# Kernel optimization log

Measured on AMD Instinct MI355X. Metric: run time of the kernel, lower is better.

## Reference

```python
import jax, jax.numpy as jnp
import numpy as np

E = 131072   # total messages
N = 8192     # dim_size (num nodes)
D = 256      # input_dim == hidden_dim (forced by h + m add)


def setup_inputs() -> dict:
    key = jax.random.key(0)
    k1, k2, k3, k4, k5 = jax.random.split(key, 5)
    msg = jax.random.normal(k1, (E, D), dtype=jnp.float32)
    index = jax.random.randint(k2, (E,), 0, N)
    t = jax.random.uniform(k3, (E,), dtype=jnp.float32)
    # torch.nn.Linear(D, D) params (kaiming-uniform-ish scale)
    W = jax.random.normal(k4, (D, D), dtype=jnp.float32) / np.sqrt(D)
    b = (jax.random.normal(k5, (D,), dtype=jnp.float32) * 0.01)
    return {"msg": msg, "index": index, "t": t, "dim_size": N, "W": W, "b": b}


def reference(msg, index, t, dim_size, W, b):
    # Original: for each node, sort its messages by t, then run the linear
    # recurrence h <- W @ (m + h) + b starting from h = 0; nodes with no
    # messages keep h = 0. Vectorized: one global stable sort by (index, t),
    # then a single segmented lax.scan with reset at segment boundaries.
    num_msgs, d = msg.shape
    order = jnp.lexsort((t, index))          # primary key: index, secondary: t
    m_sorted = msg[order]                     # [E, d]
    seg = index[order]                        # [E]

    def step(carry, inp):
        h, prev = carry
        m, s = inp
        h_in = jnp.where(s == prev, h, jnp.zeros_like(h))  # reset at new segment
        h_new = (m + h_in) @ W.T + b
        return (h_new, s), h_new

    init = (jnp.zeros((d,), msg.dtype), jnp.asarray(-1, seg.dtype))
    _, ys = jax.lax.scan(step, init, (m_sorted, seg))      # ys: [E, d]

    # final hidden per node = h at the last message of its segment
    pos = jnp.arange(num_msgs)
    last = jax.ops.segment_max(pos, seg, num_segments=dim_size)
    counts = jax.ops.segment_sum(jnp.ones((num_msgs,), jnp.int32), seg,
                                 num_segments=dim_size)
    gathered = ys[jnp.clip(last, 0, num_msgs - 1)]          # [N, d]
    hidden = jnp.where((counts > 0)[:, None], gathered, jnp.zeros_like(gathered))
    return hidden
```

## Files before the change

### kernel.cpp

```cpp
#include <hip/hip_runtime.h>
#include <hip/hip_bf16.h>

#define E_MSGS 131072
#define N_NODES 8192
#define D_DIM 256
#define XA_STRIDE 264

typedef __bf16 bf16x8 __attribute__((ext_vector_type(8)));
typedef float f32x4 __attribute__((ext_vector_type(4)));

#define BAR() asm volatile("s_waitcnt lgkmcnt(0)\n\ts_barrier" ::: "memory")


__global__ void k_scatter(const int* __restrict__ index, int* __restrict__ cursors,
                          int* __restrict__ pad) {
    int e = blockIdx.x * blockDim.x + threadIdx.x;
    int n = index[e];
    int p = atomicAdd(&cursors[n], 1);
    if (p < 64) pad[(n << 6) + p] = e;
}

__global__ void k_perm(const int* __restrict__ counts, int* __restrict__ perm) {
    __shared__ int hist[65];
    __shared__ int hcur[65];
    int tid = threadIdx.x;
    if (tid < 65) hist[tid] = 0;
    __syncthreads();
    int myc[32];
#pragma unroll
    for (int i = 0; i < 32; i++) {
        int c = min(counts[tid * 32 + i], 64);
        myc[i] = c;
        atomicAdd(&hist[c], 1);
    }
    __syncthreads();
    if (tid == 0) {
        int run = 0;
        for (int c = 64; c >= 0; c--) { hcur[c] = run; run += hist[c]; }
    }
    __syncthreads();
#pragma unroll
    for (int i = 0; i < 32; i++) {
        int pos = atomicAdd(&hcur[myc[i]], 1);
        perm[pos] = tid * 32 + i;
    }
}

__global__ void k_sortseg(const float* __restrict__ t, const int* __restrict__ counts,
                          int* __restrict__ pad) {
    int wid = (blockIdx.x * 256 + threadIdx.x) >> 6;
    int ln = threadIdx.x & 63;
    int cnt = min(counts[wid], 64);
    int base = wid << 6;
    int e = 0; float tv = 0.f;
    if (ln < cnt) { e = pad[base + ln]; tv = t[e]; }
    int rank = 0;
    for (int j = 0; j < cnt; j++) {
        float tj = __shfl(tv, j);
        int ej = __shfl(e, j);
        rank += (tj < tv) || (tj == tv && ej < e);
    }
    if (ln < cnt) pad[base + rank] = e;
}


__launch_bounds__(512, 4)
__global__ void k_gru(const float* __restrict__ msg, const float* __restrict__ W,
                      const float* __restrict__ b, const int* __restrict__ counts,
                      const int* __restrict__ spad, const int* __restrict__ perm,
                      float* __restrict__ out) {
    __shared__ __bf16 xA[2][16 * XA_STRIDE];

    int tid  = threadIdx.x;
    int wave = tid >> 6;
    int lane = tid & 63;
    int q    = lane >> 4;
    int l    = lane & 15;
    int node0 = blockIdx.x * 16;

    bf16x8 wf[8][2];
#pragma unroll
    for (int t4 = 0; t4 < 2; t4++) {
        const float* wr = W + (32 * wave + 16 * t4 + l) * D_DIM;
#pragma unroll
        for (int c = 0; c < 8; c++) {
            int k0 = 32 * c + 8 * q;
            float4 w0 = *(const float4*)(wr + k0);
            float4 w1 = *(const float4*)(wr + k0 + 4);
            bf16x8 f;
            f[0] = (__bf16)w0.x; f[1] = (__bf16)w0.y; f[2] = (__bf16)w0.z; f[3] = (__bf16)w0.w;
            f[4] = (__bf16)w1.x; f[5] = (__bf16)w1.y; f[6] = (__bf16)w1.z; f[7] = (__bf16)w1.w;
            wf[c][t4] = f;
        }
    }
    float bias[2];
#pragma unroll
    for (int t4 = 0; t4 < 2; t4++) bias[t4] = b[32 * wave + 16 * t4 + l];

    int base4[4], cnt4[4];
#pragma unroll
    for (int r = 0; r < 4; r++) {
        int n = perm[node0 + 4 * q + r];
        base4[r] = n << 6;
        cnt4[r] = min(counts[n], 64);
    }
    int S = min(counts[perm[node0]], 64);

    float h[2][4];
#pragma unroll
    for (int t4 = 0; t4 < 2; t4++)
#pragma unroll
        for (int r = 0; r < 4; r++) h[t4][r] = 0.f;

    float mvA[4][2], mvB[4][2];
    int sidp[4];
#pragma unroll
    for (int r = 0; r < 4; r++) {
        int s0 = spad[base4[r]];
        int s1 = spad[base4[r] + 1];
        const float* m0 = msg + (long)s0 * D_DIM;
        const float* m1 = msg + (long)s1 * D_DIM;
#pragma unroll
        for (int t4 = 0; t4 < 2; t4++) {
            int col = 32 * wave + 16 * t4 + l;
            xA[0][(4 * q + r) * XA_STRIDE + col] = (__bf16)m0[col];
            mvA[r][t4] = m1[col];
        }
        sidp[r] = spad[base4[r] + 2];
    }
    BAR();

    auto step = [&](int s, float (&cur)[4][2], float (&nxt)[4][2]) {
#pragma unroll
        for (int r = 0; r < 4; r++) {
            const float* mrow = msg + (long)sidp[r] * D_DIM;
#pragma unroll
            for (int t4 = 0; t4 < 2; t4++) nxt[r][t4] = mrow[32 * wave + 16 * t4 + l];
        }
#pragma unroll
        for (int r = 0; r < 4; r++)
            sidp[r] = spad[base4[r] + min(s + 3, 63)];

        const __bf16* buf = xA[s & 1];
        f32x4 acc[2];
#pragma unroll
        for (int t4 = 0; t4 < 2; t4++) acc[t4] = (f32x4){0.f, 0.f, 0.f, 0.f};
#pragma unroll
        for (int c = 0; c < 8; c++) {
            bf16x8 a = *(const bf16x8*)(buf + l * XA_STRIDE + 32 * c + 8 * q);
#pragma unroll
            for (int t4 = 0; t4 < 2; t4++)
                acc[t4] = __builtin_amdgcn_mfma_f32_16x16x32_bf16(a, wf[c][t4], acc[t4], 0, 0, 0);
        }

        __bf16* nbuf = xA[(s + 1) & 1];
#pragma unroll
        for (int t4 = 0; t4 < 2; t4++) {
#pragma unroll
            for (int r = 0; r < 4; r++) {
                float hn = acc[t4][r] + bias[t4];
                bool valid = s < cnt4[r];
                h[t4][r] = valid ? hn : h[t4][r];
                nbuf[(4 * q + r) * XA_STRIDE + 32 * wave + 16 * t4 + l] =
                    (__bf16)(h[t4][r] + cur[r][t4]);
            }
        }
        BAR();
    };

    int s = 0;
    while (s < S) {
        step(s, mvA, mvB);
        s++;
        if (s >= S) break;
        step(s, mvB, mvA);
        s++;
    }

#pragma unroll
    for (int r = 0; r < 4; r++) {
        int n = perm[node0 + 4 * q + r];
#pragma unroll
        for (int t4 = 0; t4 < 2; t4++)
            out[(long)n * D_DIM + 32 * wave + 16 * t4 + l] = h[t4][r];
    }
}


extern "C" void kernel_launch(void* const* d_in, const int* in_sizes, int n_in,
                              void* d_out, int out_size, void* d_ws, size_t ws_size,
                              hipStream_t stream) {
    const float* msg   = (const float*)d_in[0];
    const int*   index = (const int*)d_in[1];
    const float* t     = (const float*)d_in[2];
    const float* W     = (const float*)d_in[4];
    const float* b     = (const float*)d_in[5];
    float* out = (float*)d_out;

    int* ws = (int*)d_ws;
    int* cursors = ws;
    int* pad     = ws + 8192;
    int* perm    = ws + 8192 + 8192 * 64;

    hipMemsetAsync(cursors, 0, (8192 + 8192 * 64) * sizeof(int), stream);

    k_scatter<<<E_MSGS / 256, 256, 0, stream>>>(index, cursors, pad);
    k_perm<<<1, 256, 0, stream>>>(cursors, perm);
    k_sortseg<<<N_NODES * 64 / 256, 256, 0, stream>>>(t, cursors, pad);
    k_gru<<<N_NODES / 16, 512, 0, stream>>>(msg, W, b, cursors, pad, perm, out);
}
```

Measured before the change: 250.4 us.

## Unroll recurrence two steps at a time using precomputed W squared

Precomputes V = W·W and c2 = W·b + b in a prep kernel that is merged with the permutation kernel. The GRU kernel then advances two messages per step as h'' = V(h+m1) + W m2 + c2, with a prologue step for odd-length segments. This halves the number of serial barrier-separated steps along the dependency chain, in exchange for twice the MFMA work per step, double the weight registers (launch bounds lowered to 2 blocks) and extra bf16 rounding from the squared matrix.

```diff
diff --git a/kernel.cpp b/kernel.cpp
--- a/kernel.cpp
+++ b/kernel.cpp
@@ -20,29 +20,52 @@
     if (p < 64) pad[(n << 6) + p] = e;
 }
 
-__global__ void k_perm(const int* __restrict__ counts, int* __restrict__ perm) {
-    __shared__ int hist[65];
-    __shared__ int hcur[65];
+__global__ void k_prep2(const float* __restrict__ W, const float* __restrict__ b,
+                        const int* __restrict__ counts, float* __restrict__ V,
+                        float* __restrict__ c2, int* __restrict__ perm) {
     int tid = threadIdx.x;
-    if (tid < 65) hist[tid] = 0;
-    __syncthreads();
-    int myc[32];
-#pragma unroll
-    for (int i = 0; i < 32; i++) {
-        int c = min(counts[tid * 32 + i], 64);
-        myc[i] = c;
-        atomicAdd(&hist[c], 1);
-    }
-    __syncthreads();
-    if (tid == 0) {
-        int run = 0;
-        for (int c = 64; c >= 0; c--) { hcur[c] = run; run += hist[c]; }
-    }
-    __syncthreads();
-#pragma unroll
-    for (int i = 0; i < 32; i++) {
-        int pos = atomicAdd(&hcur[myc[i]], 1);
-        perm[pos] = tid * 32 + i;
+    if (blockIdx.x < 256) {
+        int i = blockIdx.x, j = tid;
+        __shared__ float red[256];
+        red[j] = W[i * 256 + j] * b[j];
+        __syncthreads();
+        for (int s = 128; s > 0; s >>= 1) {
+            if (j < s) red[j] += red[j + s];
+            __syncthreads();
+        }
+        if (j == 0) c2[i] = red[0] + b[i];
+        float acc = 0.f;
+        for (int k = 0; k < 256; k += 4) {
+            float4 wi = *(const float4*)(W + i * 256 + k);
+            acc += wi.x * W[(k + 0) * 256 + j];
+            acc += wi.y * W[(k + 1) * 256 + j];
+            acc += wi.z * W[(k + 2) * 256 + j];
+            acc += wi.w * W[(k + 3) * 256 + j];
+        }
+        V[i * 256 + j] = acc;
+    } else {
+        __shared__ int hist[65];
+        __shared__ int hcur[65];
+        if (tid < 65) hist[tid] = 0;
+        __syncthreads();
+        int myc[32];
+#pragma unroll
+        for (int i = 0; i < 32; i++) {
+            int c = min(counts[tid * 32 + i], 64);
+            myc[i] = c;
+            atomicAdd(&hist[c], 1);
+        }
+        __syncthreads();
+        if (tid == 0) {
+            int run = 0;
+            for (int c = 64; c >= 0; c--) { hcur[c] = run; run += hist[c]; }
+        }
+        __syncthreads();
+#pragma unroll
+        for (int i = 0; i < 32; i++) {
+            int pos = atomicAdd(&hcur[myc[i]], 1);
+            perm[pos] = tid * 32 + i;
+        }
     }
 }
 
@@ -64,24 +87,25 @@
 }
 
 
-__launch_bounds__(512, 4)
-__global__ void k_gru(const float* __restrict__ msg, const float* __restrict__ W,
-                      const float* __restrict__ b, const int* __restrict__ counts,
-                      const int* __restrict__ spad, const int* __restrict__ perm,
-                      float* __restrict__ out) {
-    __shared__ __bf16 xA[2][16 * XA_STRIDE];
+__launch_bounds__(512, 2)
+__global__ void k_gru2(const float* __restrict__ msg, const float* __restrict__ W,
+                       const float* __restrict__ V, const float* __restrict__ b,
+                       const float* __restrict__ c2, const int* __restrict__ counts,
+                       const int* __restrict__ spad, const int* __restrict__ perm,
+                       float* __restrict__ out) {
+    __shared__ __bf16 xB[2][16 * XA_STRIDE];
+    __shared__ __bf16 yB[2][16 * XA_STRIDE];
 
     int tid  = threadIdx.x;
-    int wave = tid >> 6;
-    int lane = tid & 63;
-    int q    = lane >> 4;
-    int l    = lane & 15;
+    int wave = tid >> 6, lane = tid & 63, q = lane >> 4, l = lane & 15;
     int node0 = blockIdx.x * 16;
-
-    bf16x8 wf[8][2];
-#pragma unroll
-    for (int t4 = 0; t4 < 2; t4++) {
-        const float* wr = W + (32 * wave + 16 * t4 + l) * D_DIM;
+    int col[2] = {32 * wave + l, 32 * wave + 16 + l};
+
+    bf16x8 wfW[8][2], wfV[8][2];
+#pragma unroll
+    for (int t = 0; t < 2; t++) {
+        const float* wr = W + (long)col[t] * D_DIM;
+        const float* vr = V + (long)col[t] * D_DIM;
 #pragma unroll
         for (int c = 0; c < 8; c++) {
             int k0 = 32 * c + 8 * q;
@@ -90,99 +114,154 @@
             bf16x8 f;
             f[0] = (__bf16)w0.x; f[1] = (__bf16)w0.y; f[2] = (__bf16)w0.z; f[3] = (__bf16)w0.w;
             f[4] = (__bf16)w1.x; f[5] = (__bf16)w1.y; f[6] = (__bf16)w1.z; f[7] = (__bf16)w1.w;
-            wf[c][t4] = f;
-        }
-    }
-    float bias[2];
-#pragma unroll
-    for (int t4 = 0; t4 < 2; t4++) bias[t4] = b[32 * wave + 16 * t4 + l];
-
-    int base4[4], cnt4[4];
+            wfW[c][t] = f;
+            float4 v0 = *(const float4*)(vr + k0);
+            float4 v1 = *(const float4*)(vr + k0 + 4);
+            bf16x8 g;
+            g[0] = (__bf16)v0.x; g[1] = (__bf16)v0.y; g[2] = (__bf16)v0.z; g[3] = (__bf16)v0.w;
+            g[4] = (__bf16)v1.x; g[5] = (__bf16)v1.y; g[6] = (__bf16)v1.z; g[7] = (__bf16)v1.w;
+            wfV[c][t] = g;
+        }
+    }
+    float bias[2]  = {b[col[0]], b[col[1]]};
+    float bias2[2] = {c2[col[0]], c2[col[1]]};
+
+    int base4[4], o4[4], dlim[4];
 #pragma unroll
     for (int r = 0; r < 4; r++) {
         int n = perm[node0 + 4 * q + r];
         base4[r] = n << 6;
-        cnt4[r] = min(counts[n], 64);
-    }
-    int S = min(counts[perm[node0]], 64);
-
+        int c = min(counts[n], 64);
+        o4[r] = c & 1;
+        dlim[r] = (c - o4[r]) >> 1;
+    }
+    int D = min(counts[perm[node0]], 64) >> 1;
+
+    float m_pro[4][2], mx0[4][2], my0[4][2], mA[4][2], mA2[4][2];
+    __bf16 mB[4][2], mB2[4][2];
+    int sidN[4][2];
+#pragma unroll
+    for (int r = 0; r < 4; r++) {
+        int o = o4[r];
+        int s_pro = spad[base4[r]];
+        int sx = spad[base4[r] + o];
+        int sy = spad[base4[r] + o + 1];
+        int sA = spad[base4[r] + o + 2];
+        int sB = spad[base4[r] + o + 3];
+        const float* mp = msg + (long)s_pro * D_DIM;
+        const float* mx = msg + (long)sx * D_DIM;
+        const float* my = msg + (long)sy * D_DIM;
+        const float* ma = msg + (long)sA * D_DIM;
+        const float* mb = msg + (long)sB * D_DIM;
+#pragma unroll
+        for (int t = 0; t < 2; t++) {
+            m_pro[r][t] = mp[col[t]];
+            mx0[r][t]   = mx[col[t]];
+            my0[r][t]   = my[col[t]];
+            mA[r][t]    = ma[col[t]];
+            mB[r][t]    = (__bf16)mb[col[t]];
+        }
+        sidN[r][0] = spad[base4[r] + min(o + 4, 63)];
+        sidN[r][1] = spad[base4[r] + min(o + 5, 63)];
+    }
+#pragma unroll
+    for (int t = 0; t < 2; t++)
+#pragma unroll
+        for (int r = 0; r < 4; r++)
+            xB[0][(4 * q + r) * XA_STRIDE + col[t]] = (__bf16)m_pro[r][t];
+    BAR();
+    f32x4 accP[2];
+#pragma unroll
+    for (int t = 0; t < 2; t++) accP[t] = (f32x4){0.f, 0.f, 0.f, 0.f};
+#pragma unroll
+    for (int c = 0; c < 8; c++) {
+        bf16x8 a = *(const bf16x8*)(&xB[0][0] + l * XA_STRIDE + 32 * c + 8 * q);
+#pragma unroll
+        for (int t = 0; t < 2; t++)
+            accP[t] = __builtin_amdgcn_mfma_f32_16x16x32_bf16(a, wfW[c][t], accP[t], 0, 0, 0);
+    }
     float h[2][4];
 #pragma unroll
-    for (int t4 = 0; t4 < 2; t4++)
-#pragma unroll
-        for (int r = 0; r < 4; r++) h[t4][r] = 0.f;
-
-    float mvA[4][2], mvB[4][2];
-    int sidp[4];
-#pragma unroll
-    for (int r = 0; r < 4; r++) {
-        int s0 = spad[base4[r]];
-        int s1 = spad[base4[r] + 1];
-        const float* m0 = msg + (long)s0 * D_DIM;
-        const float* m1 = msg + (long)s1 * D_DIM;
-#pragma unroll
-        for (int t4 = 0; t4 < 2; t4++) {
-            int col = 32 * wave + 16 * t4 + l;
-            xA[0][(4 * q + r) * XA_STRIDE + col] = (__bf16)m0[col];
-            mvA[r][t4] = m1[col];
-        }
-        sidp[r] = spad[base4[r] + 2];
-    }
+    for (int t = 0; t < 2; t++)
+#pragma unroll
+        for (int r = 0; r < 4; r++)
+            h[t][r] = o4[r] ? (accP[t][r] + bias[t]) : 0.f;
+#pragma unroll
+    for (int t = 0; t < 2; t++)
+#pragma unroll
+        for (int r = 0; r < 4; r++) {
+            xB[1][(4 * q + r) * XA_STRIDE + col[t]] = (__bf16)(h[t][r] + mx0[r][t]);
+            yB[1][(4 * q + r) * XA_STRIDE + col[t]] = (__bf16)my0[r][t];
+        }
     BAR();
 
-    auto step = [&](int s, float (&cur)[4][2], float (&nxt)[4][2]) {
+    auto dstep = [&](int d, float (&cA)[4][2], __bf16 (&cB)[4][2],
+                     float (&nA)[4][2], __bf16 (&nB)[4][2]) {
 #pragma unroll
         for (int r = 0; r < 4; r++) {
-            const float* mrow = msg + (long)sidp[r] * D_DIM;
-#pragma unroll
-            for (int t4 = 0; t4 < 2; t4++) nxt[r][t4] = mrow[32 * wave + 16 * t4 + l];
-        }
-#pragma unroll
-        for (int r = 0; r < 4; r++)
-            sidp[r] = spad[base4[r] + min(s + 3, 63)];
-
-        const __bf16* buf = xA[s & 1];
-        f32x4 acc[2];
-#pragma unroll
-        for (int t4 = 0; t4 < 2; t4++) acc[t4] = (f32x4){0.f, 0.f, 0.f, 0.f};
+            const float* ma = msg + (long)sidN[r][0] * D_DIM;
+            const float* mb = msg + (long)sidN[r][1] * D_DIM;
+#pragma unroll
+            for (int t = 0; t < 2; t++) {
+                nA[r][t] = ma[col[t]];
+                nB[r][t] = (__bf16)mb[col[t]];
+            }
+        }
+#pragma unroll
+        for (int r = 0; r < 4; r++) {
+            sidN[r][0] = spad[base4[r] + min(o4[r] + 2 * d + 6, 63)];
+            sidN[r][1] = spad[base4[r] + min(o4[r] + 2 * d + 7, 63)];
+        }
+        int rb = (d + 1) & 1, wb = d & 1;
+        f32x4 accX[2], accY[2];
+#pragma unroll
+        for (int t = 0; t < 2; t++) {
+            accX[t] = (f32x4){0.f, 0.f, 0.f, 0.f};
+            accY[t] = (f32x4){0.f, 0.f, 0.f, 0.f};
+        }
 #pragma unroll
         for (int c = 0; c < 8; c++) {
-            bf16x8 a = *(const bf16x8*)(buf + l * XA_STRIDE + 32 * c + 8 * q);
-#pragma unroll
-            for (int t4 = 0; t4 < 2; t4++)
-                acc[t4] = __builtin_amdgcn_mfma_f32_16x16x32_bf16(a, wf[c][t4], acc[t4], 0, 0, 0);
-        }
-
-        __bf16* nbuf = xA[(s + 1) & 1];
-#pragma unroll
-        for (int t4 = 0; t4 < 2; t4++) {
+            bf16x8 ax = *(const bf16x8*)(&xB[rb][0] + l * XA_STRIDE + 32 * c + 8 * q);
+#pragma unroll
+            for (int t = 0; t < 2; t++)
+                accX[t] = __builtin_amdgcn_mfma_f32_16x16x32_bf16(ax, wfV[c][t], accX[t], 0, 0, 0);
+        }
+#pragma unroll
+        for (int c = 0; c < 8; c++) {
+            bf16x8 ay = *(const bf16x8*)(&yB[rb][0] + l * XA_STRIDE + 32 * c + 8 * q);
+#pragma unroll
+            for (int t = 0; t < 2; t++)
+                accY[t] = __builtin_amdgcn_mfma_f32_16x16x32_bf16(ay, wfW[c][t], accY[t], 0, 0, 0);
+        }
+#pragma unroll
+        for (int t = 0; t < 2; t++) {
 #pragma unroll
             for (int r = 0; r < 4; r++) {
-                float hn = acc[t4][r] + bias[t4];
-                bool valid = s < cnt4[r];
-                h[t4][r] = valid ? hn : h[t4][r];
-                nbuf[(4 * q + r) * XA_STRIDE + 32 * wave + 16 * t4 + l] =
-                    (__bf16)(h[t4][r] + cur[r][t4]);
+                float hn = accX[t][r] + accY[t][r] + bias2[t];
+                bool valid = d < dlim[r];
+                h[t][r] = valid ? hn : h[t][r];
+                xB[wb][(4 * q + r) * XA_STRIDE + col[t]] = (__bf16)(h[t][r] + cA[r][t]);
+                yB[wb][(4 * q + r) * XA_STRIDE + col[t]] = cB[r][t];
             }
         }
         BAR();
     };
 
-    int s = 0;
-    while (s < S) {
-        step(s, mvA, mvB);
-        s++;
-        if (s >= S) break;
-        step(s, mvB, mvA);
-        s++;
+    int d = 0;
+    while (d < D) {
+        dstep(d, mA, mB, mA2, mB2);
+        d++;
+        if (d >= D) break;
+        dstep(d, mA2, mB2, mA, mB);
+        d++;
     }
 
 #pragma unroll
     for (int r = 0; r < 4; r++) {
         int n = perm[node0 + 4 * q + r];
 #pragma unroll
-        for (int t4 = 0; t4 < 2; t4++)
-            out[(long)n * D_DIM + 32 * wave + 16 * t4 + l] = h[t4][r];
+        for (int t = 0; t < 2; t++)
+            out[(long)n * D_DIM + col[t]] = h[t][r];
     }
 }
 
@@ -201,11 +280,13 @@
     int* cursors = ws;
     int* pad     = ws + 8192;
     int* perm    = ws + 8192 + 8192 * 64;
+    float* V     = (float*)(perm + 8192);
+    float* c2    = V + 65536;
 
     hipMemsetAsync(cursors, 0, (8192 + 8192 * 64) * sizeof(int), stream);
 
     k_scatter<<<E_MSGS / 256, 256, 0, stream>>>(index, cursors, pad);
-    k_perm<<<1, 256, 0, stream>>>(cursors, perm);
+    k_prep2<<<257, 256, 0, stream>>>(W, b, cursors, V, c2, perm);
     k_sortseg<<<N_NODES * 64 / 256, 256, 0, stream>>>(t, cursors, pad);
-    k_gru<<<N_NODES / 16, 512, 0, stream>>>(msg, W, b, cursors, pad, perm, out);
-}
+    k_gru2<<<N_NODES / 16, 512, 0, stream>>>(msg, W, V, b, c2, cursors, pad, perm, out);
+}
```

Measured after the change: 255.6 us. +2.1%, slower.

## Fuse sort and perm kernels; stage messages in LDS via vectorized triple buffer

Applied to the files above, without the earlier changes.

Merges the per-node sort and the histogram permutation kernels into one launch, where an extra block computes the permutation, removing one kernel launch. In the GRU kernel, message rows are now loaded with coalesced float4 reads, where each lane owns 8 contiguous columns of one row, instead of scalar strided loads. They are converted to bf16 and written into a third LDS buffer, and the m+h add reads the message back from LDS. This cuts global load instructions and register-held prefetch state, at the cost of more LDS traffic, extra LDS capacity and a read-modify-write on the shared buffer.

```diff
diff --git a/kernel.cpp b/kernel.cpp
--- a/kernel.cpp
+++ b/kernel.cpp
@@ -20,47 +20,47 @@
     if (p < 64) pad[(n << 6) + p] = e;
 }
 
-__global__ void k_perm(const int* __restrict__ counts, int* __restrict__ perm) {
-    __shared__ int hist[65];
-    __shared__ int hcur[65];
+__global__ void k_sortperm(const float* __restrict__ t, const int* __restrict__ counts,
+                           int* __restrict__ pad, int* __restrict__ perm) {
     int tid = threadIdx.x;
-    if (tid < 65) hist[tid] = 0;
-    __syncthreads();
-    int myc[32];
-#pragma unroll
-    for (int i = 0; i < 32; i++) {
-        int c = min(counts[tid * 32 + i], 64);
-        myc[i] = c;
-        atomicAdd(&hist[c], 1);
-    }
-    __syncthreads();
-    if (tid == 0) {
-        int run = 0;
-        for (int c = 64; c >= 0; c--) { hcur[c] = run; run += hist[c]; }
-    }
-    __syncthreads();
-#pragma unroll
-    for (int i = 0; i < 32; i++) {
-        int pos = atomicAdd(&hcur[myc[i]], 1);
-        perm[pos] = tid * 32 + i;
-    }
-}
-
-__global__ void k_sortseg(const float* __restrict__ t, const int* __restrict__ counts,
-                          int* __restrict__ pad) {
-    int wid = (blockIdx.x * 256 + threadIdx.x) >> 6;
-    int ln = threadIdx.x & 63;
-    int cnt = min(counts[wid], 64);
-    int base = wid << 6;
-    int e = 0; float tv = 0.f;
-    if (ln < cnt) { e = pad[base + ln]; tv = t[e]; }
-    int rank = 0;
-    for (int j = 0; j < cnt; j++) {
-        float tj = __shfl(tv, j);
-        int ej = __shfl(e, j);
-        rank += (tj < tv) || (tj == tv && ej < e);
-    }
-    if (ln < cnt) pad[base + rank] = e;
+    if (blockIdx.x < 2048) {
+        int wid = (blockIdx.x * 256 + tid) >> 6;
+        int ln = tid & 63;
+        int cnt = min(counts[wid], 64);
+        int base = wid << 6;
+        int e = 0; float tv = 0.f;
+        if (ln < cnt) { e = pad[base + ln]; tv = t[e]; }
+        int rank = 0;
+        for (int j = 0; j < cnt; j++) {
+            float tj = __shfl(tv, j);
+            int ej = __shfl(e, j);
+            rank += (tj < tv) || (tj == tv && ej < e);
+        }
+        if (ln < cnt) pad[base + rank] = e;
+    } else {
+        __shared__ int hist[65];
+        __shared__ int hcur[65];
+        if (tid < 65) hist[tid] = 0;
+        __syncthreads();
+        int myc[32];
+#pragma unroll
+        for (int i = 0; i < 32; i++) {
+            int c = min(counts[tid * 32 + i], 64);
+            myc[i] = c;
+            atomicAdd(&hist[c], 1);
+        }
+        __syncthreads();
+        if (tid == 0) {
+            int run = 0;
+            for (int c = 64; c >= 0; c--) { hcur[c] = run; run += hist[c]; }
+        }
+        __syncthreads();
+#pragma unroll
+        for (int i = 0; i < 32; i++) {
+            int pos = atomicAdd(&hcur[myc[i]], 1);
+            perm[pos] = tid * 32 + i;
+        }
+    }
 }
 
 
@@ -69,7 +69,7 @@
                       const float* __restrict__ b, const int* __restrict__ counts,
                       const int* __restrict__ spad, const int* __restrict__ perm,
                       float* __restrict__ out) {
-    __shared__ __bf16 xA[2][16 * XA_STRIDE];
+    __shared__ __bf16 xA[3][16 * XA_STRIDE];
 
     int tid  = threadIdx.x;
     int wave = tid >> 6;
@@ -97,51 +97,58 @@
 #pragma unroll
     for (int t4 = 0; t4 < 2; t4++) bias[t4] = b[32 * wave + 16 * t4 + l];
 
-    int base4[4], cnt4[4];
-#pragma unroll
-    for (int r = 0; r < 4; r++) {
-        int n = perm[node0 + 4 * q + r];
-        base4[r] = n << 6;
-        cnt4[r] = min(counts[n], 64);
-    }
+    int cnt4[4];
+#pragma unroll
+    for (int r = 0; r < 4; r++) cnt4[r] = min(counts[perm[node0 + 4 * q + r]], 64);
     int S = min(counts[perm[node0]], 64);
 
+    int jrow = lane >> 2;
+    int k4 = lane & 3;
+    long baseL = (long)perm[node0 + jrow] << 6;
+    int colL = 32 * wave + 8 * k4;
+
     float h[2][4];
 #pragma unroll
     for (int t4 = 0; t4 < 2; t4++)
 #pragma unroll
         for (int r = 0; r < 4; r++) h[t4][r] = 0.f;
 
-    float mvA[4][2], mvB[4][2];
-    int sidp[4];
-#pragma unroll
-    for (int r = 0; r < 4; r++) {
-        int s0 = spad[base4[r]];
-        int s1 = spad[base4[r] + 1];
-        const float* m0 = msg + (long)s0 * D_DIM;
-        const float* m1 = msg + (long)s1 * D_DIM;
-#pragma unroll
-        for (int t4 = 0; t4 < 2; t4++) {
-            int col = 32 * wave + 16 * t4 + l;
-            xA[0][(4 * q + r) * XA_STRIDE + col] = (__bf16)m0[col];
-            mvA[r][t4] = m1[col];
-        }
-        sidp[r] = spad[base4[r] + 2];
+    int sid0 = spad[baseL + 0];
+    int sid1 = spad[baseL + 1];
+    int sid2 = spad[baseL + 2];
+    int sidR = spad[baseL + 3];
+    float4 mf0, mf1;
+    {
+        const float* m0 = msg + (long)sid0 * D_DIM + colL;
+        const float* m1 = msg + (long)sid1 * D_DIM + colL;
+        const float* m2 = msg + (long)sid2 * D_DIM + colL;
+        float4 a0 = *(const float4*)m0, a1 = *(const float4*)(m0 + 4);
+        float4 b0 = *(const float4*)m1, b1 = *(const float4*)(m1 + 4);
+        mf0 = *(const float4*)m2; mf1 = *(const float4*)(m2 + 4);
+        bf16x8 fa, fb;
+        fa[0] = (__bf16)a0.x; fa[1] = (__bf16)a0.y; fa[2] = (__bf16)a0.z; fa[3] = (__bf16)a0.w;
+        fa[4] = (__bf16)a1.x; fa[5] = (__bf16)a1.y; fa[6] = (__bf16)a1.z; fa[7] = (__bf16)a1.w;
+        fb[0] = (__bf16)b0.x; fb[1] = (__bf16)b0.y; fb[2] = (__bf16)b0.z; fb[3] = (__bf16)b0.w;
+        fb[4] = (__bf16)b1.x; fb[5] = (__bf16)b1.y; fb[6] = (__bf16)b1.z; fb[7] = (__bf16)b1.w;
+        *(bf16x8*)(&xA[0][jrow * XA_STRIDE + colL]) = fa;
+        *(bf16x8*)(&xA[1][jrow * XA_STRIDE + colL]) = fb;
     }
     BAR();
 
-    auto step = [&](int s, float (&cur)[4][2], float (&nxt)[4][2]) {
-#pragma unroll
-        for (int r = 0; r < 4; r++) {
-            const float* mrow = msg + (long)sidp[r] * D_DIM;
-#pragma unroll
-            for (int t4 = 0; t4 < 2; t4++) nxt[r][t4] = mrow[32 * wave + 16 * t4 + l];
-        }
-#pragma unroll
-        for (int r = 0; r < 4; r++)
-            sidp[r] = spad[base4[r] + min(s + 3, 63)];
-
-        const __bf16* buf = xA[s & 1];
+    auto step = [&](int s, int rb, int hb, int mb) {
+        {
+            bf16x8 f;
+            f[0] = (__bf16)mf0.x; f[1] = (__bf16)mf0.y; f[2] = (__bf16)mf0.z; f[3] = (__bf16)mf0.w;
+            f[4] = (__bf16)mf1.x; f[5] = (__bf16)mf1.y; f[6] = (__bf16)mf1.z; f[7] = (__bf16)mf1.w;
+            *(bf16x8*)(&xA[mb][jrow * XA_STRIDE + colL]) = f;
+        }
+        {
+            const float* mrow = msg + (long)sidR * D_DIM + colL;
+            mf0 = *(const float4*)mrow;
+            mf1 = *(const float4*)(mrow + 4);
+            sidR = spad[baseL + min(s + 4, 63)];
+        }
+        const __bf16* buf = xA[rb];
         f32x4 acc[2];
 #pragma unroll
         for (int t4 = 0; t4 < 2; t4++) acc[t4] = (f32x4){0.f, 0.f, 0.f, 0.f};
@@ -152,8 +159,6 @@
             for (int t4 = 0; t4 < 2; t4++)
                 acc[t4] = __builtin_amdgcn_mfma_f32_16x16x32_bf16(a, wf[c][t4], acc[t4], 0, 0, 0);
         }
-
-        __bf16* nbuf = xA[(s + 1) & 1];
 #pragma unroll
         for (int t4 = 0; t4 < 2; t4++) {
 #pragma unroll
@@ -161,20 +166,19 @@
                 float hn = acc[t4][r] + bias[t4];
                 bool valid = s < cnt4[r];
                 h[t4][r] = valid ? hn : h[t4][r];
-                nbuf[(4 * q + r) * XA_STRIDE + 32 * wave + 16 * t4 + l] =
-                    (__bf16)(h[t4][r] + cur[r][t4]);
+                int off = (4 * q + r) * XA_STRIDE + 32 * wave + 16 * t4 + l;
+                float mval = (float)xA[hb][off];
+                xA[hb][off] = (__bf16)(h[t4][r] + mval);
             }
         }
         BAR();
     };
 
     int s = 0;
-    while (s < S) {
-        step(s, mvA, mvB);
-        s++;
-        if (s >= S) break;
-        step(s, mvB, mvA);
-        s++;
+    while (true) {
+        if (s >= S) break; step(s, 0, 1, 2); s++;
+        if (s >= S) break; step(s, 1, 2, 0); s++;
+        if (s >= S) break; step(s, 2, 0, 1); s++;
     }
 
 #pragma unroll
@@ -205,7 +209,6 @@
     hipMemsetAsync(cursors, 0, (8192 + 8192 * 64) * sizeof(int), stream);
 
     k_scatter<<<E_MSGS / 256, 256, 0, stream>>>(index, cursors, pad);
-    k_perm<<<1, 256, 0, stream>>>(cursors, perm);
-    k_sortseg<<<N_NODES * 64 / 256, 256, 0, stream>>>(t, cursors, pad);
+    k_sortperm<<<2049, 256, 0, stream>>>(t, cursors, pad, perm);
     k_gru<<<N_NODES / 16, 512, 0, stream>>>(msg, W, b, cursors, pad, perm, out);
 }
```

Result: no change. 249.2 us (-0.5%).
